# Kernel optimization log

Hardware: AMD Instinct MI355X
Metric: run time of the kernel (lower is better)

Reference implementation:

```python
import jax, jax.numpy as jnp
import numpy as np

T, B, D = 512, 16, 1024


def entmax_1_5(x):
    # x: [..., D] fp32. 1.5-entmax via sort + cumsum threshold search.
    x = x - jnp.max(x, axis=-1, keepdims=True)
    x_sorted = jnp.sort(x, axis=-1)[..., ::-1]          # descending
    cumsum = jnp.cumsum(x_sorted, axis=-1)
    d = x.shape[-1]
    k = jnp.arange(1, d + 1, dtype=x.dtype)
    tau = (cumsum - 1.0) / k                             # [..., D]
    support = x_sorted >= tau
    k_star = jnp.clip(jnp.sum(support, axis=-1, keepdims=True), 1, None)
    tau_star = jnp.take_along_axis(tau, k_star - 1, axis=-1)
    p_unnorm = jnp.sqrt(jnp.clip(x - tau_star, 0.0, None))  # (.)**0.5
    return p_unnorm / (jnp.sum(p_unnorm, axis=-1, keepdims=True) + 1e-10)


def setup_inputs() -> dict:
    key = jax.random.key(0)
    k1, k2, k3, k4 = jax.random.split(key, 4)
    x = jax.random.normal(k1, (T, B, D), dtype=jnp.float32)
    z = jax.random.normal(k2, (T, B, D), dtype=jnp.float32)
    h0 = jnp.zeros((B, D), dtype=jnp.float32)
    # parameters (xavier-ish scale for W_x, scaled near-orthogonal-ish for W_h)
    W_x = jax.random.normal(k3, (D, D), dtype=jnp.float32) * (1.0 / np.sqrt(D))
    W_h = jax.random.normal(k4, (D, D), dtype=jnp.float32) * (0.9 / np.sqrt(D))
    b = jnp.zeros((D,), dtype=jnp.float32)
    return {"x": x, "z": z, "h0": h0, "W_x": W_x, "W_h": W_h, "b": b}


def reference(x, z, h0, W_x, W_h, b):
    # gate does not depend on the recurrence -> compute for all T at once
    gate = entmax_1_5(z.astype(jnp.float32)).astype(z.dtype)  # [T,B,D]

    def step(h_prev, x_t):
        h_new = jnp.tanh(x_t @ W_x.T + h_prev @ W_h.T + b)
        return h_new, h_new

    _, hs = jax.lax.scan(step, h0, x)          # hs: [T,B,D]
    h = jnp.concatenate([h0[None], hs], axis=0)  # [T+1,B,D]
    output = hs * gate                           # [T,B,D]
    return (output, h)
```

## Files before the change

kernel.cpp:

```cpp
#include <hip/hip_runtime.h>
#include <math.h>

#define T_STEPS 512
#define BATCH   16
#define DIM     1024
#define M_TOTAL (T_STEPS*BATCH)
#define OUT_SEC ((size_t)M_TOTAL*DIM)
#define BD      (BATCH*DIM)

#define TAG_BYTES ((size_t)2*BD*8)

#define NB_GEMM 512
#define NB_GATE 2048

__device__ __forceinline__ float wred64(float v){
  #pragma unroll
  for (int off = 32; off >= 1; off >>= 1) v += __shfl_xor(v, off, 64);
  return v;
}

#define KA(v) asm volatile("" : "+v"(v.x), "+v"(v.y), "+v"(v.z), "+v"(v.w))

__global__ __launch_bounds__(256) void prep_kernel(const float* __restrict__ X,
                                                   const float* __restrict__ Wx,
                                                   const float* __restrict__ bias,
                                                   float* __restrict__ out_h,
                                                   const float* __restrict__ z,
                                                   float* __restrict__ gate_out){
  __shared__ float As[8][128];
  __shared__ float Bs[8][128];
  const int tid = threadIdx.x;

  if (blockIdx.x < NB_GEMM){
    const int bm = blockIdx.x >> 3;
    const int bn = blockIdx.x & 7;
    const int m0 = bm*128, n0 = bn*128;
    const int tx = tid & 15, ty = tid >> 4;
    const int sm = tid >> 1;
    const int sk = (tid & 1) * 4;

    float acc[8][8] = {};

    const float* Xp = X  + (size_t)(m0+sm)*DIM + sk;
    const float* Wp = Wx + (size_t)(n0+sm)*DIM + sk;

    float4 av = *reinterpret_cast<const float4*>(Xp);
    float4 wv = *reinterpret_cast<const float4*>(Wp);

    for (int k0 = 0; k0 < DIM; k0 += 8){
      __syncthreads();
      As[sk+0][sm]=av.x; As[sk+1][sm]=av.y; As[sk+2][sm]=av.z; As[sk+3][sm]=av.w;
      Bs[sk+0][sm]=wv.x; Bs[sk+1][sm]=wv.y; Bs[sk+2][sm]=wv.z; Bs[sk+3][sm]=wv.w;
      const int kn = (k0 + 8 < DIM) ? (k0 + 8) : 0;
      const float4 av2 = *reinterpret_cast<const float4*>(Xp + kn);
      const float4 wv2 = *reinterpret_cast<const float4*>(Wp + kn);
      __syncthreads();
      #pragma unroll
      for (int k = 0; k < 8; ++k){
        float af[8], bf[8];
        #pragma unroll
        for (int i = 0; i < 8; ++i) af[i] = As[k][ty + 16*i];
        #pragma unroll
        for (int j = 0; j < 8; ++j) bf[j] = Bs[k][tx + 16*j];
        #pragma unroll
        for (int i = 0; i < 8; ++i)
          #pragma unroll
          for (int j = 0; j < 8; ++j) acc[i][j] = fmaf(af[i], bf[j], acc[i][j]);
      }
      av = av2; wv = wv2;
    }

    float bv[8];
    #pragma unroll
    for (int j = 0; j < 8; ++j) bv[j] = bias[n0 + tx + 16*j];
    #pragma unroll
    for (int i = 0; i < 8; ++i){
      float* dst = out_h + (size_t)(m0 + ty + 16*i + BATCH)*DIM + n0 + tx;
      #pragma unroll
      for (int j = 0; j < 8; ++j) dst[16*j] = acc[i][j] + bv[j];
    }
  } else {
    const int gb   = blockIdx.x - NB_GEMM;
    const int row  = gb * 4 + (tid >> 6);
    const int lane = tid & 63;
    const float* zr = z + (size_t)row * DIM;

    float x[16];
    #pragma unroll
    for (int e = 0; e < 4; ++e){
      float4 v = *reinterpret_cast<const float4*>(zr + e*256 + lane*4);
      x[e*4+0]=v.x; x[e*4+1]=v.y; x[e*4+2]=v.z; x[e*4+3]=v.w;
    }

    float m = x[0];
    #pragma unroll
    for (int i = 1; i < 16; ++i) m = fmaxf(m, x[i]);
    #pragma unroll
    for (int off = 32; off >= 1; off >>= 1) m = fmaxf(m, __shfl_xor(m, off, 64));

    float lo = m - 1.0f, hi = m;
    for (int it = 0; it < 30; ++it){
      float mid = 0.5f*(lo + hi);
      float f = 0.f;
      #pragma unroll
      for (int i = 0; i < 16; ++i) f += fmaxf(x[i] - mid, 0.f);
      f = wred64(f);
      if (f >= 1.0f) lo = mid; else hi = mid;
    }
    float s = 0.f, kc = 0.f;
    #pragma unroll
    for (int i = 0; i < 16; ++i){ if (x[i] > lo){ s += x[i]; kc += 1.f; } }
    s = wred64(s); kc = wred64(kc);
    const float tau = (s - 1.0f) / kc;

    float p[16]; float ps = 0.f;
    #pragma unroll
    for (int i = 0; i < 16; ++i){ p[i] = sqrtf(fmaxf(x[i] - tau, 0.f)); ps += p[i]; }
    ps = wred64(ps);
    const float inv = 1.0f / (ps + 1e-10f);

    float* go = gate_out + (size_t)row * DIM;
    #pragma unroll
    for (int e = 0; e < 4; ++e){
      float4 v; v.x=p[e*4]*inv; v.y=p[e*4+1]*inv; v.z=p[e*4+2]*inv; v.w=p[e*4+3]*inv;
      *reinterpret_cast<float4*>(go + e*256 + lane*4) = v;
    }
  }
}

__global__ __launch_bounds__(512, 1) void rnn_tag(const float* __restrict__ h0,
                                                  const float* __restrict__ Wh,
                                                  float* __restrict__ out,
                                                  uint2* __restrict__ tagbuf){
  float* out_h = out + OUT_SEC;
  const int tid  = threadIdx.x;
  const int lane = tid & 63;
  const int w    = tid >> 6;
  const int b    = blockIdx.x >> 4;
  const int s    = blockIdx.x & 15;
  const int dbase = s*64 + w*8;

  __shared__ float hbuf[2][DIM];

  float4 wreg[8][4];
  #pragma unroll
  for (int r = 0; r < 8; ++r)
    #pragma unroll
    for (int j = 0; j < 4; ++j)
      wreg[r][j] = *reinterpret_cast<const float4*>(
          Wh + (size_t)(dbase + r)*DIM + lane*4 + j*256);

  KA(wreg[0][0]); KA(wreg[0][1]); KA(wreg[0][2]); KA(wreg[0][3]);
  KA(wreg[1][0]); KA(wreg[1][1]); KA(wreg[1][2]); KA(wreg[1][3]);
  KA(wreg[2][0]); KA(wreg[2][1]); KA(wreg[2][2]); KA(wreg[2][3]);
  KA(wreg[3][0]); KA(wreg[3][1]); KA(wreg[3][2]); KA(wreg[3][3]);
  KA(wreg[4][0]); KA(wreg[4][1]); KA(wreg[4][2]); KA(wreg[4][3]);
  KA(wreg[5][0]); KA(wreg[5][1]); KA(wreg[5][2]); KA(wreg[5][3]);
  KA(wreg[6][0]); KA(wreg[6][1]); KA(wreg[6][2]); KA(wreg[6][3]);
  KA(wreg[7][0]); KA(wreg[7][1]); KA(wreg[7][2]); KA(wreg[7][3]);

  if (tid < 16)
    reinterpret_cast<float4*>(out_h + (size_t)b*DIM + s*64)[tid] =
        reinterpret_cast<const float4*>(h0 + (size_t)b*DIM + s*64)[tid];

  const int myrow   = lane >> 3;
  const bool active = ((lane & 7) == 0);

  for (int t = 0; t < T_STEPS; ++t){
    float pre_v = 0.f, gate_v = 0.f;
    if (active){
      const size_t d = dbase + myrow;
      pre_v  = out_h[(size_t)(t+1)*BD + (size_t)b*DIM + d];
      gate_v = out  [(size_t)t*BD     + (size_t)b*DIM + d];
    }

    if (t == 0){
      const float2 hl = *reinterpret_cast<const float2*>(h0 + (size_t)b*DIM + 2*tid);
      *reinterpret_cast<float2*>(&hbuf[0][2*tid]) = hl;
    } else {
      const uint2* pp = tagbuf + (size_t)(t & 1)*BD + (size_t)b*DIM + 2*tid;
      const unsigned want = (unsigned)t;
      float4 q;
      do {
        asm volatile("global_load_dwordx4 %0, %1, off sc0 sc1\n\t"
                     "s_waitcnt vmcnt(0)"
                     : "=&v"(q) : "v"(pp) : "memory");
      } while (__float_as_uint(q.y) != want || __float_as_uint(q.w) != want);
      *reinterpret_cast<float2*>(&hbuf[t & 1][2*tid]) = make_float2(q.x, q.z);
    }
    __syncthreads();

    const float* src = &hbuf[t & 1][0];
    const float4 hv0 = *reinterpret_cast<const float4*>(src + lane*4);
    const float4 hv1 = *reinterpret_cast<const float4*>(src + 256 + lane*4);
    const float4 hv2 = *reinterpret_cast<const float4*>(src + 512 + lane*4);
    const float4 hv3 = *reinterpret_cast<const float4*>(src + 768 + lane*4);

    float v0,v1,v2,v3,v4,v5,v6,v7;
    {
      #define DOTROW(R, OUTV)                                            \
        { const float4 w0=wreg[R][0], w1=wreg[R][1],                     \
                       w2=wreg[R][2], w3=wreg[R][3];                     \
          float a_ = 0.f;                                                \
          a_ = fmaf(w0.x,hv0.x,fmaf(w0.y,hv0.y,fmaf(w0.z,hv0.z,fmaf(w0.w,hv0.w,a_)))); \
          a_ = fmaf(w1.x,hv1.x,fmaf(w1.y,hv1.y,fmaf(w1.z,hv1.z,fmaf(w1.w,hv1.w,a_)))); \
          a_ = fmaf(w2.x,hv2.x,fmaf(w2.y,hv2.y,fmaf(w2.z,hv2.z,fmaf(w2.w,hv2.w,a_)))); \
          a_ = fmaf(w3.x,hv3.x,fmaf(w3.y,hv3.y,fmaf(w3.z,hv3.z,fmaf(w3.w,hv3.w,a_)))); \
          OUTV = a_; }
      DOTROW(0,v0) DOTROW(1,v1) DOTROW(2,v2) DOTROW(3,v3)
      DOTROW(4,v4) DOTROW(5,v5) DOTROW(6,v6) DOTROW(7,v7)
      #undef DOTROW
    }

    const bool sA = (lane & 32) != 0;
    float a0 = (sA? v4 : v0) + __shfl_xor(sA? v0 : v4, 32, 64);
    float a1 = (sA? v5 : v1) + __shfl_xor(sA? v1 : v5, 32, 64);
    float a2 = (sA? v6 : v2) + __shfl_xor(sA? v2 : v6, 32, 64);
    float a3 = (sA? v7 : v3) + __shfl_xor(sA? v3 : v7, 32, 64);
    const bool sB = (lane & 16) != 0;
    float b0 = (sB? a2 : a0) + __shfl_xor(sB? a0 : a2, 16, 64);
    float b1 = (sB? a3 : a1) + __shfl_xor(sB? a1 : a3, 16, 64);
    const bool sC = (lane & 8) != 0;
    float c0 = (sC? b1 : b0) + __shfl_xor(sC? b0 : b1, 8, 64);
    c0 += __shfl_xor(c0, 4, 64);
    c0 += __shfl_xor(c0, 2, 64);
    c0 += __shfl_xor(c0, 1, 64);

    if (active){
      const float v  = pre_v + c0;
      const float e  = __expf(2.0f * v);
      const float hn = 1.0f - 2.0f / (e + 1.0f);
      const size_t d = dbase + myrow;
      if (t != T_STEPS - 1){
        const unsigned long long pkt =
            ((unsigned long long)(unsigned)(t + 1) << 32) |
            (unsigned long long)__float_as_uint(hn);
        __hip_atomic_store(
            reinterpret_cast<unsigned long long*>(
                tagbuf + (size_t)((t + 1) & 1)*BD + (size_t)b*DIM + d),
            pkt, __ATOMIC_RELAXED, __HIP_MEMORY_SCOPE_AGENT);
      }
      out_h[(size_t)(t+1)*BD + (size_t)b*DIM + d] = hn;
      out  [(size_t)t*BD     + (size_t)b*DIM + d] = hn * gate_v;
    }
  }
}

extern "C" void kernel_launch(void* const* d_in, const int* in_sizes, int n_in,
                              void* d_out, int out_size, void* d_ws, size_t ws_size,
                              hipStream_t stream){
  (void)in_sizes; (void)n_in; (void)out_size; (void)ws_size;
  const float* x    = (const float*)d_in[0];
  const float* z    = (const float*)d_in[1];
  const float* h0   = (const float*)d_in[2];
  const float* Wx   = (const float*)d_in[3];
  const float* Wh   = (const float*)d_in[4];
  const float* bias = (const float*)d_in[5];
  float* out   = (float*)d_out;
  float* out_h = out + OUT_SEC;

  hipMemsetAsync(d_ws, 0, TAG_BYTES, stream);
  prep_kernel<<<NB_GEMM + NB_GATE, 256, 0, stream>>>(x, Wx, bias, out_h, z, out);
  rnn_tag    <<<256, 512, 0, stream>>>(h0, Wh, out, (uint2*)d_ws);
}
```

Before: 1.100 ms.

## Add dual-path tag exchange with workgroup-scope fast buffer and remap block-to-batch

The recurrent kernel now publishes each new hidden value twice: once to a fast buffer with workgroup-scope store and once to the authoritative agent-scope buffer. Consumers poll both with different cache bits and accept whichever carries the right step tag, to cut cross-block handoff latency when blocks happen to share a cache. The block index mapping is also swapped so the 16 blocks of one batch row are spread differently across CUs/XCDs. This adds extra stores and loads per step, and correctness of the fast path depends on stale-tag detection.

```diff
diff --git a/kernel.cpp b/kernel.cpp
--- a/kernel.cpp
+++ b/kernel.cpp
@@ -8,7 +8,9 @@
 #define OUT_SEC ((size_t)M_TOTAL*DIM)
 #define BD      (BATCH*DIM)
 
-#define TAG_BYTES ((size_t)2*BD*8)
+#define TAG_UNITS   ((size_t)2*BD)
+#define AUTH_BYTES  (TAG_UNITS*8)
+#define DUAL_BYTES  (TAG_UNITS*8*2)
 
 #define NB_GEMM 512
 #define NB_GATE 2048
@@ -128,16 +130,18 @@
   }
 }
 
+template<bool DUAL>
 __global__ __launch_bounds__(512, 1) void rnn_tag(const float* __restrict__ h0,
                                                   const float* __restrict__ Wh,
                                                   float* __restrict__ out,
-                                                  uint2* __restrict__ tagbuf){
+                                                  uint2* __restrict__ fastbuf,
+                                                  uint2* __restrict__ authbuf){
   float* out_h = out + OUT_SEC;
   const int tid  = threadIdx.x;
   const int lane = tid & 63;
   const int w    = tid >> 6;
-  const int b    = blockIdx.x >> 4;
-  const int s    = blockIdx.x & 15;
+  const int b    = blockIdx.x & 15;
+  const int s    = blockIdx.x >> 4;
   const int dbase = s*64 + w*8;
 
   __shared__ float hbuf[2][DIM];
@@ -178,15 +182,34 @@
       const float2 hl = *reinterpret_cast<const float2*>(h0 + (size_t)b*DIM + 2*tid);
       *reinterpret_cast<float2*>(&hbuf[0][2*tid]) = hl;
     } else {
-      const uint2* pp = tagbuf + (size_t)(t & 1)*BD + (size_t)b*DIM + 2*tid;
+      const size_t off = (size_t)(t & 1)*BD + (size_t)b*DIM + 2*tid;
       const unsigned want = (unsigned)t;
-      float4 q;
-      do {
-        asm volatile("global_load_dwordx4 %0, %1, off sc0 sc1\n\t"
-                     "s_waitcnt vmcnt(0)"
-                     : "=&v"(q) : "v"(pp) : "memory");
-      } while (__float_as_uint(q.y) != want || __float_as_uint(q.w) != want);
-      *reinterpret_cast<float2*>(&hbuf[t & 1][2*tid]) = make_float2(q.x, q.z);
+      if constexpr (DUAL){
+        const uint2* pf = fastbuf + off;
+        const uint2* pa = authbuf + off;
+        float4 f, a;
+        for (;;){
+          asm volatile("global_load_dwordx4 %0, %2, off sc0\n\t"
+                       "global_load_dwordx4 %1, %3, off sc0 sc1\n\t"
+                       "s_waitcnt vmcnt(0)"
+                       : "=&v"(f), "=&v"(a) : "v"(pf), "v"(pa) : "memory");
+          const bool ok0 = (__float_as_uint(f.y)==want) | (__float_as_uint(a.y)==want);
+          const bool ok1 = (__float_as_uint(f.w)==want) | (__float_as_uint(a.w)==want);
+          if (ok0 & ok1) break;
+        }
+        const float v0 = (__float_as_uint(f.y)==want) ? f.x : a.x;
+        const float v1 = (__float_as_uint(f.w)==want) ? f.z : a.z;
+        *reinterpret_cast<float2*>(&hbuf[t & 1][2*tid]) = make_float2(v0, v1);
+      } else {
+        const uint2* pp = authbuf + off;
+        float4 q;
+        do {
+          asm volatile("global_load_dwordx4 %0, %1, off sc0 sc1\n\t"
+                       "s_waitcnt vmcnt(0)"
+                       : "=&v"(q) : "v"(pp) : "memory");
+        } while (__float_as_uint(q.y) != want || __float_as_uint(q.w) != want);
+        *reinterpret_cast<float2*>(&hbuf[t & 1][2*tid]) = make_float2(q.x, q.z);
+      }
     }
     __syncthreads();
 
@@ -235,9 +258,14 @@
         const unsigned long long pkt =
             ((unsigned long long)(unsigned)(t + 1) << 32) |
             (unsigned long long)__float_as_uint(hn);
+        const size_t doff = (size_t)((t + 1) & 1)*BD + (size_t)b*DIM + d;
+        if constexpr (DUAL){
+          __hip_atomic_store(
+              reinterpret_cast<unsigned long long*>(fastbuf + doff),
+              pkt, __ATOMIC_RELAXED, __HIP_MEMORY_SCOPE_WORKGROUP);
+        }
         __hip_atomic_store(
-            reinterpret_cast<unsigned long long*>(
-                tagbuf + (size_t)((t + 1) & 1)*BD + (size_t)b*DIM + d),
+            reinterpret_cast<unsigned long long*>(authbuf + doff),
             pkt, __ATOMIC_RELAXED, __HIP_MEMORY_SCOPE_AGENT);
       }
       out_h[(size_t)(t+1)*BD + (size_t)b*DIM + d] = hn;
@@ -249,7 +277,7 @@
 extern "C" void kernel_launch(void* const* d_in, const int* in_sizes, int n_in,
                               void* d_out, int out_size, void* d_ws, size_t ws_size,
                               hipStream_t stream){
-  (void)in_sizes; (void)n_in; (void)out_size; (void)ws_size;
+  (void)in_sizes; (void)n_in; (void)out_size;
   const float* x    = (const float*)d_in[0];
   const float* z    = (const float*)d_in[1];
   const float* h0   = (const float*)d_in[2];
@@ -258,8 +286,14 @@
   const float* bias = (const float*)d_in[5];
   float* out   = (float*)d_out;
   float* out_h = out + OUT_SEC;
-
-  hipMemsetAsync(d_ws, 0, TAG_BYTES, stream);
+  uint2* fastbuf = (uint2*)d_ws;
+  uint2* authbuf = fastbuf + TAG_UNITS;
+
+  const bool dual = (ws_size >= DUAL_BYTES);
+  hipMemsetAsync(d_ws, 0, dual ? DUAL_BYTES : AUTH_BYTES, stream);
   prep_kernel<<<NB_GEMM + NB_GATE, 256, 0, stream>>>(x, Wx, bias, out_h, z, out);
-  rnn_tag    <<<256, 512, 0, stream>>>(h0, Wh, out, (uint2*)d_ws);
-}
+  if (dual)
+    rnn_tag<true ><<<256, 512, 0, stream>>>(h0, Wh, out, fastbuf, authbuf);
+  else
+    rnn_tag<false><<<256, 512, 0, stream>>>(h0, Wh, out, fastbuf, fastbuf);
+}
```

After: 1.059 ms (median of 2 runs). -3.8%, faster.
